# Kernel optimization log

Measured on AMD Instinct MI355X. Metric: run time of the kernel, lower is better.

The kernel has to match this reference:

```python
import jax, jax.numpy as jnp
import numpy as np

B, T, C = 2, 2048, 1024
H, GAMMA = 16, 8
D = C // H
SCALE = 1.0 / np.sqrt(D).astype(np.float32)


def setup_inputs() -> dict:
    key = jax.random.key(0)
    ks = jax.random.split(key, 6)
    w = 0.02
    return {
        'x': jax.random.normal(ks[0], (B, T, C), dtype=jnp.float32),
        'Wq': jax.random.normal(ks[1], (C, 2 * C), dtype=jnp.float32) * w,
        'Wk': jax.random.normal(ks[2], (C, 2 * C), dtype=jnp.float32) * w,
        'Wv': jax.random.normal(ks[3], (C, C), dtype=jnp.float32) * w,
        'Wo': jax.random.normal(ks[4], (C, C), dtype=jnp.float32) * w,
        'theta_offset': jax.random.normal(ks[5], (H,), dtype=jnp.float32) * 0.1,
    }


def _heads(t):
    # (B, T, C) -> (B, H, T, D)
    return t.reshape(B, T, H, D).transpose(0, 2, 1, 3)


def reference(x, Wq, Wk, Wv, Wo, theta_offset):
    q_raw = x @ Wq                      # (B, T, 2C)
    k_raw = x @ Wk                      # (B, T, 2C)
    v = _heads(x @ Wv)                  # (B, H, T, D)

    q_amp, q_phase = jnp.split(q_raw, 2, axis=-1)
    k_amp, k_phase = jnp.split(k_raw, 2, axis=-1)
    q_amp = jax.nn.softplus(_heads(q_amp))
    q_phase = _heads(q_phase)
    k_amp = jax.nn.softplus(_heads(k_amp))
    k_phase = _heads(k_phase)

    q_real = q_amp * jnp.cos(q_phase)
    q_imag = q_amp * jnp.sin(q_phase)
    k_real = k_amp * jnp.cos(k_phase)
    k_imag = k_amp * jnp.sin(k_phase)

    scores = (jnp.einsum('bhtd,bhsd->bhts', q_real, k_real)
              + jnp.einsum('bhtd,bhsd->bhts', q_imag, k_imag)) * SCALE

    # theta gating (active since T > GAMMA)
    cycle_ids = jnp.arange(T, dtype=jnp.float32) / GAMMA
    cycle_dist = cycle_ids[None, :] - cycle_ids[:, None]        # (T, T)
    theta_gate = jnp.cos(theta_offset[:, None, None] * cycle_dist)  # (H, T, T)
    scores = scores * theta_gate[None]

    causal = jnp.tril(jnp.ones((T, T), dtype=bool))
    scores = jnp.where(causal[None, None], scores, -jnp.inf)
    attn = jax.nn.softmax(scores, axis=-1)

    out = jnp.einsum('bhts,bhsd->bhtd', attn, v)
    out = out.transpose(0, 2, 1, 3).reshape(B, T, C)
    return out @ Wo
```

## Files before the change

kernel.cpp:

```cpp
#include <hip/hip_runtime.h>
#include <hip/hip_bf16.h>
#include <math.h>

#define Bc 2
#define Tc 2048
#define Cc 1024
#define Hc 16
#define Dc 64

typedef __attribute__((ext_vector_type(8))) short short8;
typedef __attribute__((ext_vector_type(4))) float f32x4;

#define L2E 1.44269504088896f
#define SM_M 20.0f

__device__ __forceinline__ short f2bf(float x) {
    unsigned u = __float_as_uint(x);
    u += 0x7fff + ((u >> 16) & 1);
    return (short)(u >> 16);
}
__device__ __forceinline__ unsigned pack2bf_fast(float a, float b) {
    unsigned ua = __float_as_uint(a) + 0x8000u;
    unsigned ub = __float_as_uint(b) + 0x8000u;
    return __builtin_amdgcn_perm(ub, ua, 0x07060302);
}
__device__ __forceinline__ float softplus_fast(float a) {
    return fmaxf(a, 0.f) + __logf(1.f + __expf(-fabsf(a)));
}

template <int EPI>
__global__ __launch_bounds__(256) void gemm_bt_mfma(
    const short* __restrict__ A, const short* __restrict__ Bt,
    float* __restrict__ Cf, short* __restrict__ Cb, short* __restrict__ Cb2,
    int M, int N, int K)
{
    __shared__ __attribute__((aligned(16))) short As[128 * 32];
    __shared__ __attribute__((aligned(16))) short Bs[128 * 32];

    const int tid = threadIdx.x;
    const int wave = tid >> 6, lane = tid & 63;
    const int quad = lane >> 4, c = lane & 15;
    const int wm = wave >> 1, wn = wave & 1;
    const int m0 = blockIdx.y * 128, n0 = blockIdx.x * 128;

    const int srow = lane >> 2;
    const int scol = (lane & 3) * 8;
    const short* Ag = A  + (size_t)(m0 + wave * 32 + srow) * K + scol;
    const short* Bg = Bt + (size_t)(n0 + wave * 32 + srow) * K + scol;
    short* AsW = As + (wave * 32) * 32;
    short* BsW = Bs + (wave * 32) * 32;

    f32x4 acc[4][4];
#pragma unroll
    for (int i = 0; i < 4; ++i)
#pragma unroll
        for (int j = 0; j < 4; ++j)
            acc[i][j] = (f32x4){0.f, 0.f, 0.f, 0.f};

    for (int k0 = 0; k0 < K; k0 += 32) {
        __syncthreads();
#pragma unroll
        for (int i = 0; i < 2; ++i) {
            __builtin_amdgcn_global_load_lds(
                (const __attribute__((address_space(1))) void*)(Ag + k0 + (size_t)i * 16 * K),
                (__attribute__((address_space(3))) void*)(AsW + i * 16 * 32), 16, 0, 0);
            __builtin_amdgcn_global_load_lds(
                (const __attribute__((address_space(1))) void*)(Bg + k0 + (size_t)i * 16 * K),
                (__attribute__((address_space(3))) void*)(BsW + i * 16 * 32), 16, 0, 0);
        }
        __syncthreads();

        short8 af[4], bf[4];
#pragma unroll
        for (int mt = 0; mt < 4; ++mt)
            af[mt] = *(const short8*)&As[(wm * 64 + mt * 16 + c) * 32 + quad * 8];
#pragma unroll
        for (int nt = 0; nt < 4; ++nt)
            bf[nt] = *(const short8*)&Bs[(wn * 64 + nt * 16 + c) * 32 + quad * 8];
#pragma unroll
        for (int mt = 0; mt < 4; ++mt)
#pragma unroll
            for (int nt = 0; nt < 4; ++nt)
                acc[mt][nt] = __builtin_amdgcn_mfma_f32_16x16x32_bf16(
                    af[mt], bf[nt], acc[mt][nt], 0, 0, 0);
    }

    if (EPI == 2) {
        const int g = n0 >> 7;
        const int isK = g >> 4;
        const int h = g & 15;
        const float scl = isK ? 1.f : 0.125f;
        short* dst = isK ? Cb2 : Cb;
#pragma unroll
        for (int mt = 0; mt < 4; ++mt) {
#pragma unroll
            for (int reg = 0; reg < 4; ++reg) {
                int m = m0 + wm * 64 + mt * 16 + quad * 4 + reg;
                int bb = m >> 11, tt = m & (Tc - 1);
                size_t base = (((size_t)bb * Hc + h) * Tc + tt) * 128;
#pragma unroll
                for (int nt = 0; nt < 2; ++nt) {
                    float amp = acc[mt][nt][reg];
                    float ph  = acc[mt][nt + 2][reg];
                    int d = wn * 32 + nt * 16 + c;
                    float sp = softplus_fast(amp) * scl;
                    float sn, cs;
                    __sincosf(ph, &sn, &cs);
                    dst[base + d]      = f2bf(sp * cs);
                    dst[base + d + 64] = f2bf(sp * sn);
                }
            }
        }
    } else {
#pragma unroll
        for (int mt = 0; mt < 4; ++mt) {
#pragma unroll
            for (int reg = 0; reg < 4; ++reg) {
                size_t row = m0 + wm * 64 + mt * 16 + quad * 4 + reg;
#pragma unroll
                for (int nt = 0; nt < 4; ++nt) {
                    size_t col = n0 + wn * 64 + nt * 16 + c;
                    if (EPI == 1) Cb[row * N + col] = f2bf(acc[mt][nt][reg]);
                    else          Cf[row * N + col] = acc[mt][nt][reg];
                }
            }
        }
    }
}

__global__ __launch_bounds__(256) void gemm_v2t(
    const short* __restrict__ A, const short* __restrict__ Bt,
    short* __restrict__ v2t)
{
    __shared__ __attribute__((aligned(16))) short As[128 * 32];
    __shared__ __attribute__((aligned(16))) short Bs[128 * 32];
    __shared__ __attribute__((aligned(16))) short tile[128 * 136];

    const int K = Cc;
    const int tid = threadIdx.x;
    const int wave = tid >> 6, lane = tid & 63;
    const int quad = lane >> 4, c = lane & 15;
    const int wm = wave >> 1, wn = wave & 1;
    const int m0 = blockIdx.y * 128, n0 = blockIdx.x * 128;

    const int srow = lane >> 2;
    const int scol = (lane & 3) * 8;
    const short* Ag = A  + (size_t)(m0 + wave * 32 + srow) * K + scol;
    const short* Bg = Bt + (size_t)(n0 + wave * 32 + srow) * K + scol;
    short* AsW = As + (wave * 32) * 32;
    short* BsW = Bs + (wave * 32) * 32;

    f32x4 acc[4][4];
#pragma unroll
    for (int i = 0; i < 4; ++i)
#pragma unroll
        for (int j = 0; j < 4; ++j)
            acc[i][j] = (f32x4){0.f, 0.f, 0.f, 0.f};

    for (int k0 = 0; k0 < K; k0 += 32) {
        __syncthreads();
#pragma unroll
        for (int i = 0; i < 2; ++i) {
            __builtin_amdgcn_global_load_lds(
                (const __attribute__((address_space(1))) void*)(Ag + k0 + (size_t)i * 16 * K),
                (__attribute__((address_space(3))) void*)(AsW + i * 16 * 32), 16, 0, 0);
            __builtin_amdgcn_global_load_lds(
                (const __attribute__((address_space(1))) void*)(Bg + k0 + (size_t)i * 16 * K),
                (__attribute__((address_space(3))) void*)(BsW + i * 16 * 32), 16, 0, 0);
        }
        __syncthreads();

        short8 af[4], bf[4];
#pragma unroll
        for (int mt = 0; mt < 4; ++mt)
            af[mt] = *(const short8*)&As[(wm * 64 + mt * 16 + c) * 32 + quad * 8];
#pragma unroll
        for (int nt = 0; nt < 4; ++nt)
            bf[nt] = *(const short8*)&Bs[(wn * 64 + nt * 16 + c) * 32 + quad * 8];
#pragma unroll
        for (int mt = 0; mt < 4; ++mt)
#pragma unroll
            for (int nt = 0; nt < 4; ++nt)
                acc[mt][nt] = __builtin_amdgcn_mfma_f32_16x16x32_bf16(
                    af[mt], bf[nt], acc[mt][nt], 0, 0, 0);
    }

#pragma unroll
    for (int mt = 0; mt < 4; ++mt)
#pragma unroll
        for (int reg = 0; reg < 4; ++reg) {
            int tl = wm * 64 + mt * 16 + quad * 4 + reg;
#pragma unroll
            for (int nt = 0; nt < 4; ++nt)
                tile[(wn * 64 + nt * 16 + c) * 136 + tl] = f2bf(acc[mt][nt][reg]);
        }
    __syncthreads();

    const int b = m0 >> 11, tl0 = m0 & (Tc - 1);
#pragma unroll
    for (int i = 0; i < 8; ++i) {
        int n = i * 16 + (tid >> 4);
        int t8 = (tid & 15) * 8;
        int ng = n0 + n, h = ng >> 6, d = ng & 63;
        *(short8*)&v2t[(((size_t)b * Hc + h) * Dc + d) * Tc + tl0 + t8] =
            *(const short8*)&tile[n * 136 + t8];
    }
}

__global__ __launch_bounds__(256) void xconv(const float* __restrict__ x,
                                             short* __restrict__ xb)
{
    int idx = blockIdx.x * 256 + threadIdx.x;
    float4 v = *(const float4*)&x[(size_t)idx * 4];
    short4 o = {f2bf(v.x), f2bf(v.y), f2bf(v.z), f2bf(v.w)};
    *(short4*)&xb[(size_t)idx * 4] = o;
}

__global__ __launch_bounds__(256) void wtrans_qk(const float* __restrict__ Wq,
                                                 const float* __restrict__ Wk,
                                                 short* __restrict__ Bt)
{
    __shared__ short tile[64][80];
    const int n0 = blockIdx.x * 64, k0 = blockIdx.y * 64;
    const int half = blockIdx.z;
    const float* W = half ? Wk : Wq;
    const int tid = threadIdx.x;
#pragma unroll
    for (int i = 0; i < 4; ++i) {
        int e = i * 256 + tid;
        int k = e >> 4, n4 = (e & 15) * 4;
        float4 v = *(const float4*)&W[(size_t)(k0 + k) * 2048 + n0 + n4];
        tile[k][n4]     = f2bf(v.x);
        tile[k][n4 + 1] = f2bf(v.y);
        tile[k][n4 + 2] = f2bf(v.z);
        tile[k][n4 + 3] = f2bf(v.w);
    }
    __syncthreads();
#pragma unroll
    for (int i = 0; i < 16; ++i) {
        int e = i * 256 + tid;
        int n = e >> 6, k = e & 63;
        int ng = n0 + n;
        int sub = ng >> 10, hh = (ng >> 6) & 15, dd = ng & 63;
        int r = (half * 16 + hh) * 128 + (dd >> 5) * 64 + sub * 32 + (dd & 31);
        Bt[(size_t)r * Cc + k0 + k] = tile[k][n];
    }
}

__global__ __launch_bounds__(256) void wtrans2(const float* __restrict__ Wv,
                                               const float* __restrict__ Wo,
                                               short* __restrict__ WtBase)
{
    __shared__ short tile[64][80];
    const int n0 = blockIdx.x * 64, k0 = blockIdx.y * 64;
    const float* W = blockIdx.z ? Wo : Wv;
    short* Wt = WtBase + (size_t)blockIdx.z * Cc * Cc;
    const int tid = threadIdx.x;
#pragma unroll
    for (int i = 0; i < 4; ++i) {
        int e = i * 256 + tid;
        int k = e >> 4, n4 = (e & 15) * 4;
        float4 v = *(const float4*)&W[(size_t)(k0 + k) * Cc + n0 + n4];
        tile[k][n4]     = f2bf(v.x);
        tile[k][n4 + 1] = f2bf(v.y);
        tile[k][n4 + 2] = f2bf(v.z);
        tile[k][n4 + 3] = f2bf(v.w);
    }
    __syncthreads();
#pragma unroll
    for (int i = 0; i < 16; ++i) {
        int e = i * 256 + tid;
        int n = e >> 6, k = e & 63;
        Wt[(size_t)(n0 + n) * Cc + k0 + k] = tile[k][n];
    }
}

__global__ __launch_bounds__(512, 4) void moire_attn5(
    const short* __restrict__ q2, const short* __restrict__ k2,
    const short* __restrict__ v2t, const float* __restrict__ theta,
    short* __restrict__ att)
{
    __shared__ __attribute__((aligned(16))) short Ks[2][64 * 128];
    __shared__ __attribute__((aligned(16))) short Vt[2][64 * 64];
    __shared__ __attribute__((aligned(16))) short Ps[8][16 * 64];

    const int tid = threadIdx.x;
    const int wave = tid >> 6, lane = tid & 63;
    const int quad = lane >> 4, c = lane & 15;
    const int tx = wave >> 2, wq = wave & 3;
    const int p = blockIdx.x, h = blockIdx.y, b = blockIdx.z;
    const int qx = tx ? (31 - p) : p;
    const int q0 = qx * 64;
    const float th = theta[h];

    const short* k2b = k2 + (size_t)(b * Hc + h) * Tc * 128;
    const short* v2b = v2t + (size_t)(b * Hc + h) * Dc * Tc;

    short8 qf[4];
    const short* qp = q2 + ((size_t)(b * Hc + h) * Tc + q0 + wq * 16 + c) * 128;
#pragma unroll
    for (int i = 0; i < 4; ++i)
        qf[i] = *(const short8*)(qp + i * 32 + quad * 8);

    const int t_l = wq * 16 + c;
    float x0 = th * 0.125f * (float)(q0 + t_l);
    float cb = __cosf(x0), sb = -__sinf(x0);
    float cOff[4][4], sOff[4][4];
#pragma unroll
    for (int mt = 0; mt < 4; ++mt)
#pragma unroll
        for (int reg = 0; reg < 4; ++reg) {
            float a = th * 0.125f * (float)(mt * 16 + quad * 4 + reg);
            cOff[mt][reg] = __cosf(a) * L2E;
            sOff[mt][reg] = __sinf(a) * L2E;
        }
    const float cD = __cosf(8.f * th), sD = __sinf(8.f * th);

    f32x4 oacc[4];
    float lsum = 0.f;
#pragma unroll
    for (int nt = 0; nt < 4; ++nt)
        oacc[nt] = (f32x4){0.f, 0.f, 0.f, 0.f};

    auto stage = [&](int jts) {
        short* KsB = &Ks[jts & 1][0];
        short* VtB = &Vt[jts & 1][0];
        const int s0 = jts * 64;
#pragma unroll
        for (int i = 0; i < 2; ++i) {
            int ch = i * 512 + tid;
            int row = ch >> 4, j = ch & 15;
            const short* src = k2b + (size_t)(s0 + row) * 128 + ((j ^ (row & 15)) << 3);
            __builtin_amdgcn_global_load_lds(
                (const __attribute__((address_space(1))) void*)src,
                (__attribute__((address_space(3))) void*)(KsB + (i * 512 + wave * 64) * 8),
                16, 0, 0);
        }
        {
            int ch = tid;
            int row = ch >> 3, j = ch & 7;
            const short* src = v2b + (size_t)row * Tc + s0 + ((j ^ (row & 7)) << 3);
            __builtin_amdgcn_global_load_lds(
                (const __attribute__((address_space(1))) void*)src,
                (__attribute__((address_space(3))) void*)(VtB + (wave * 64) * 8),
                16, 0, 0);
        }
    };

    stage(0);
    const int jtEnd = 31 - p;
    for (int jt = 0; jt <= jtEnd; ++jt) {
        __syncthreads();
        if (jt < jtEnd) stage(jt + 1);

        if (jt <= qx) {
            const short* KsB = &Ks[jt & 1][0];
            const short* VtB = &Vt[jt & 1][0];
            const bool diag = (jt == qx);

            f32x4 s_acc[4];
#pragma unroll
            for (int mt = 0; mt < 4; ++mt) {
                f32x4 a = {0.f, 0.f, 0.f, 0.f};
#pragma unroll
                for (int kk = 0; kk < 4; ++kk) {
                    short8 kf = *(const short8*)&KsB[(mt * 16 + c) * 128 +
                                                     (((kk * 4 + quad) ^ c) << 3)];
                    a = __builtin_amdgcn_mfma_f32_16x16x32_bf16(kf, qf[kk], a, 0, 0, 0);
                }
                s_acc[mt] = a;
            }

#pragma unroll
            for (int mt = 0; mt < 4; ++mt) {
                float pv[4];
#pragma unroll
                for (int reg = 0; reg < 4; ++reg) {
                    float g2 = cb * cOff[mt][reg] - sb * sOff[mt][reg];
                    float arg = fmaf(s_acc[mt][reg], g2, -SM_M * L2E);
                    if (diag && (mt * 16 + quad * 4 + reg) > t_l) arg = -1e30f;
                    pv[reg] = exp2f(arg);
                }
                lsum += (pv[0] + pv[1]) + (pv[2] + pv[3]);
                uint2 pk = {pack2bf_fast(pv[0], pv[1]), pack2bf_fast(pv[2], pv[3])};
                int slot = ((mt * 2 + (quad >> 1)) ^ (c & 7));
                *(uint2*)&Ps[wave][c * 64 + slot * 8 + (quad & 1) * 4] = pk;
            }

            short8 pf[2];
#pragma unroll
            for (int kk = 0; kk < 2; ++kk)
                pf[kk] = *(const short8*)&Ps[wave][c * 64 +
                             (((kk * 4 + quad) ^ (c & 7)) << 3)];
#pragma unroll
            for (int nt = 0; nt < 4; ++nt)
#pragma unroll
                for (int kk = 0; kk < 2; ++kk) {
                    short8 vf = *(const short8*)&VtB[(nt * 16 + c) * 64 +
                                 (((kk * 4 + quad) ^ (c & 7)) << 3)];
                    oacc[nt] = __builtin_amdgcn_mfma_f32_16x16x32_bf16(
                        pf[kk], vf, oacc[nt], 0, 0, 0);
                }

            float ncb = cb * cD - sb * sD;
            sb = sb * cD + cb * sD;
            cb = ncb;
        }
    }

    float l = lsum;
    l += __shfl_xor(l, 16);
    l += __shfl_xor(l, 32);
    float il = 1.f / l;
    float ilr[4];
#pragma unroll
    for (int reg = 0; reg < 4; ++reg)
        ilr[reg] = __shfl(il, quad * 4 + reg);
#pragma unroll
    for (int reg = 0; reg < 4; ++reg) {
        int t_g = q0 + wq * 16 + quad * 4 + reg;
#pragma unroll
        for (int nt = 0; nt < 4; ++nt)
            att[(size_t)(b * Tc + t_g) * Cc + h * Dc + nt * 16 + c] =
                f2bf(oacc[nt][reg] * ilr[reg]);
    }
}

extern "C" void kernel_launch(void* const* d_in, const int* in_sizes, int n_in,
                              void* d_out, int out_size, void* d_ws, size_t ws_size,
                              hipStream_t stream)
{
    const float* x     = (const float*)d_in[0];
    const float* Wq    = (const float*)d_in[1];
    const float* Wk    = (const float*)d_in[2];
    const float* Wv    = (const float*)d_in[3];
    const float* Wo    = (const float*)d_in[4];
    const float* theta = (const float*)d_in[5];
    float* out = (float*)d_out;

    const int M = Bc * Tc;
    char* ws = (char*)d_ws;
    const size_t MB = 1 << 20;
    short* xb   = (short*)(ws);
    short* Bqk  = (short*)(ws + 8 * MB);
    short* Wvt  = (short*)(ws + 16 * MB);
    short* Wot  = (short*)(ws + 18 * MB);
    short* v2t  = (short*)(ws + 28 * MB);
    short* attb = (short*)(ws + 36 * MB);
    short* q2   = (short*)(ws + 44 * MB);
    short* k2   = (short*)d_out;

    xconv<<<(size_t)M * Cc / 1024, 256, 0, stream>>>(x, xb);
    wtrans_qk<<<dim3(2048 / 64, Cc / 64, 2), 256, 0, stream>>>(Wq, Wk, Bqk);
    wtrans2<<<dim3(Cc / 64, Cc / 64, 2), 256, 0, stream>>>(Wv, Wo, Wvt);

    gemm_bt_mfma<2><<<dim3(4096 / 128, M / 128), 256, 0, stream>>>(
        xb, Bqk, nullptr, q2, k2, M, 4096, Cc);
    gemm_v2t<<<dim3(Cc / 128, M / 128), 256, 0, stream>>>(xb, Wvt, v2t);

    moire_attn5<<<dim3(16, Hc, Bc), 512, 0, stream>>>(q2, k2, v2t, theta, attb);

    gemm_bt_mfma<0><<<dim3(Cc / 128, M / 128), 256, 0, stream>>>(
        attb, Wot, out, nullptr, nullptr, M, Cc, Cc);
}
```

Measured before the change: 264.6 us.

## Software-pipeline attention loop: defer PV matmul one tile behind QK scores

Restructures the attention main loop so each iteration runs the P·V MFMA for the previous key tile before computing scores for the current tile. V tiles are now staged one iteration later than K tiles, and a final PV step runs after the loop. The aim is to overlap the exp/softmax VALU work with MFMA work and to give V loads more time to land. The cost is more complex control flow, reliance on the per-wave Ps buffer persisting across the barrier, and an extra tail step.

```diff
diff --git a/kernel.cpp b/kernel.cpp
--- a/kernel.cpp
+++ b/kernel.cpp
@@ -275,7 +275,7 @@
     }
 }
 
-__global__ __launch_bounds__(512, 4) void moire_attn5(
+__global__ __launch_bounds__(512, 4) void moire_attn6(
     const short* __restrict__ q2, const short* __restrict__ k2,
     const short* __restrict__ v2t, const float* __restrict__ theta,
     short* __restrict__ att)
@@ -322,9 +322,8 @@
     for (int nt = 0; nt < 4; ++nt)
         oacc[nt] = (f32x4){0.f, 0.f, 0.f, 0.f};
 
-    auto stage = [&](int jts) {
+    auto stageK = [&](int jts) {
         short* KsB = &Ks[jts & 1][0];
-        short* VtB = &Vt[jts & 1][0];
         const int s0 = jts * 64;
 #pragma unroll
         for (int i = 0; i < 2; ++i) {
@@ -336,77 +335,95 @@
                 (__attribute__((address_space(3))) void*)(KsB + (i * 512 + wave * 64) * 8),
                 16, 0, 0);
         }
-        {
-            int ch = tid;
-            int row = ch >> 3, j = ch & 7;
-            const short* src = v2b + (size_t)row * Tc + s0 + ((j ^ (row & 7)) << 3);
-            __builtin_amdgcn_global_load_lds(
-                (const __attribute__((address_space(1))) void*)src,
-                (__attribute__((address_space(3))) void*)(VtB + (wave * 64) * 8),
-                16, 0, 0);
-        }
     };
-
-    stage(0);
+    auto stageV = [&](int jts) {
+        short* VtB = &Vt[jts & 1][0];
+        const int s0 = jts * 64;
+        int row = tid >> 3, j = tid & 7;
+        const short* src = v2b + (size_t)row * Tc + s0 + ((j ^ (row & 7)) << 3);
+        __builtin_amdgcn_global_load_lds(
+            (const __attribute__((address_space(1))) void*)src,
+            (__attribute__((address_space(3))) void*)(VtB + (wave * 64) * 8),
+            16, 0, 0);
+    };
+
+    auto do_pv = [&](int jprev) {
+        const short* VtB = &Vt[jprev & 1][0];
+        short8 pf[2];
+#pragma unroll
+        for (int kk = 0; kk < 2; ++kk)
+            pf[kk] = *(const short8*)&Ps[wave][c * 64 +
+                         (((kk * 4 + quad) ^ (c & 7)) << 3)];
+#pragma unroll
+        for (int nt = 0; nt < 4; ++nt)
+#pragma unroll
+            for (int kk = 0; kk < 2; ++kk) {
+                short8 vf = *(const short8*)&VtB[(nt * 16 + c) * 64 +
+                             (((kk * 4 + quad) ^ (c & 7)) << 3)];
+                oacc[nt] = __builtin_amdgcn_mfma_f32_16x16x32_bf16(
+                    pf[kk], vf, oacc[nt], 0, 0, 0);
+            }
+    };
+
+    auto do_s = [&](int jt) {
+        const short* KsB = &Ks[jt & 1][0];
+        const bool diag = (jt == qx);
+
+        f32x4 s_acc[4];
+#pragma unroll
+        for (int mt = 0; mt < 4; ++mt) {
+            f32x4 a = {0.f, 0.f, 0.f, 0.f};
+#pragma unroll
+            for (int kk = 0; kk < 4; ++kk) {
+                short8 kf = *(const short8*)&KsB[(mt * 16 + c) * 128 +
+                                                 (((kk * 4 + quad) ^ c) << 3)];
+                a = __builtin_amdgcn_mfma_f32_16x16x32_bf16(kf, qf[kk], a, 0, 0, 0);
+            }
+            s_acc[mt] = a;
+        }
+
+#pragma unroll
+        for (int mt = 0; mt < 4; ++mt) {
+            float pv[4];
+#pragma unroll
+            for (int reg = 0; reg < 4; ++reg) {
+                float g2 = cb * cOff[mt][reg] - sb * sOff[mt][reg];
+                float arg = fmaf(s_acc[mt][reg], g2, -SM_M * L2E);
+                if (diag && (mt * 16 + quad * 4 + reg) > t_l) arg = -1e30f;
+                pv[reg] = exp2f(arg);
+            }
+            lsum += (pv[0] + pv[1]) + (pv[2] + pv[3]);
+            uint2 pk = {pack2bf_fast(pv[0], pv[1]), pack2bf_fast(pv[2], pv[3])};
+            int slot = ((mt * 2 + (quad >> 1)) ^ (c & 7));
+            *(uint2*)&Ps[wave][c * 64 + slot * 8 + (quad & 1) * 4] = pk;
+        }
+
+        float ncb = cb * cD - sb * sD;
+        sb = sb * cD + cb * sD;
+        cb = ncb;
+    };
+
+    stageK(0);
     const int jtEnd = 31 - p;
     for (int jt = 0; jt <= jtEnd; ++jt) {
         __syncthreads();
-        if (jt < jtEnd) stage(jt + 1);
-
-        if (jt <= qx) {
-            const short* KsB = &Ks[jt & 1][0];
-            const short* VtB = &Vt[jt & 1][0];
-            const bool diag = (jt == qx);
-
-            f32x4 s_acc[4];
-#pragma unroll
-            for (int mt = 0; mt < 4; ++mt) {
-                f32x4 a = {0.f, 0.f, 0.f, 0.f};
-#pragma unroll
-                for (int kk = 0; kk < 4; ++kk) {
-                    short8 kf = *(const short8*)&KsB[(mt * 16 + c) * 128 +
-                                                     (((kk * 4 + quad) ^ c) << 3)];
-                    a = __builtin_amdgcn_mfma_f32_16x16x32_bf16(kf, qf[kk], a, 0, 0, 0);
-                }
-                s_acc[mt] = a;
-            }
-
-#pragma unroll
-            for (int mt = 0; mt < 4; ++mt) {
-                float pv[4];
-#pragma unroll
-                for (int reg = 0; reg < 4; ++reg) {
-                    float g2 = cb * cOff[mt][reg] - sb * sOff[mt][reg];
-                    float arg = fmaf(s_acc[mt][reg], g2, -SM_M * L2E);
-                    if (diag && (mt * 16 + quad * 4 + reg) > t_l) arg = -1e30f;
-                    pv[reg] = exp2f(arg);
-                }
-                lsum += (pv[0] + pv[1]) + (pv[2] + pv[3]);
-                uint2 pk = {pack2bf_fast(pv[0], pv[1]), pack2bf_fast(pv[2], pv[3])};
-                int slot = ((mt * 2 + (quad >> 1)) ^ (c & 7));
-                *(uint2*)&Ps[wave][c * 64 + slot * 8 + (quad & 1) * 4] = pk;
-            }
-
-            short8 pf[2];
-#pragma unroll
-            for (int kk = 0; kk < 2; ++kk)
-                pf[kk] = *(const short8*)&Ps[wave][c * 64 +
-                             (((kk * 4 + quad) ^ (c & 7)) << 3)];
-#pragma unroll
-            for (int nt = 0; nt < 4; ++nt)
-#pragma unroll
-                for (int kk = 0; kk < 2; ++kk) {
-                    short8 vf = *(const short8*)&VtB[(nt * 16 + c) * 64 +
-                                 (((kk * 4 + quad) ^ (c & 7)) << 3)];
-                    oacc[nt] = __builtin_amdgcn_mfma_f32_16x16x32_bf16(
-                        pf[kk], vf, oacc[nt], 0, 0, 0);
-                }
-
-            float ncb = cb * cD - sb * sD;
-            sb = sb * cD + cb * sD;
-            cb = ncb;
-        }
-    }
+        if (jt < jtEnd) stageK(jt + 1);
+        stageV(jt);
+
+        const bool doS  = (jt <= qx);
+        const bool doPV = (jt >= 1) & (jt <= qx + 1);
+        if (doS & doPV) {
+            do_pv(jt - 1);
+            do_s(jt);
+        } else if (doS) {
+            do_s(jt);
+        } else if (doPV) {
+            do_pv(jt - 1);
+        }
+    }
+
+    __syncthreads();
+    if (qx == jtEnd) do_pv(jtEnd);
 
     float l = lsum;
     l += __shfl_xor(l, 16);
@@ -458,7 +475,7 @@
         xb, Bqk, nullptr, q2, k2, M, 4096, Cc);
     gemm_v2t<<<dim3(Cc / 128, M / 128), 256, 0, stream>>>(xb, Wvt, v2t);
 
-    moire_attn5<<<dim3(16, Hc, Bc), 512, 0, stream>>>(q2, k2, v2t, theta, attb);
+    moire_attn6<<<dim3(16, Hc, Bc), 512, 0, stream>>>(q2, k2, v2t, theta, attb);
 
     gemm_bt_mfma<0><<<dim3(Cc / 128, M / 128), 256, 0, stream>>>(
         attb, Wot, out, nullptr, nullptr, M, Cc, Cc);
```

New measurement: 262.2 us. About the same (-0.9%).
